# Kernel tuning notes

Hardware: AMD Instinct MI355X
Metric: run time of the kernel (lower is better)

## Reference

```python
import jax, jax.numpy as jnp
import numpy as np

N = 4096            # nodes
LMAX = 6
NUM_COEF = (LMAX + 1) ** 2   # 49 SH coefficients
RES = 18            # S2 grid resolution (lat = lon = 18)
C = 128             # num_channels


def setup_inputs() -> dict:
    key = jax.random.key(0)
    k1, k2, k3, k4 = jax.random.split(key, 4)
    return {
        "inputs": jax.random.normal(k1, (N, NUM_COEF, 2 * C), dtype=jnp.float32),
        "scalars": jax.random.normal(k2, (N, 3 * C), dtype=jnp.float32),
        # SO3Grid projection matrices (precomputed SH-basis grids in the real module)
        "to_grid_mat": jax.random.normal(k3, (RES, RES, NUM_COEF), dtype=jnp.float32) / np.sqrt(NUM_COEF).astype(np.float32),
        "from_grid_mat": jax.random.normal(k4, (RES, RES, NUM_COEF), dtype=jnp.float32) / np.float32(RES),
    }


def reference(inputs, scalars, to_grid_mat, from_grid_mat):
    # inputs:  [N, (lmax+1)^2, 2C]; scalars: [N, 3C]
    n, k, c2 = inputs.shape
    s = scalars[:, None, :]                       # [N, 1, 3C]
    # Type-0 path part 1: SwiGLU on first 2C scalars -> [N, 1, C]
    a, b = jnp.split(s[..., :c2], 2, axis=-1)
    output_scalars = jax.nn.silu(a) * b
    # Type-0 path part 2: sigmoid gate on last C scalars -> [N, 1, C]
    gate_scalars = jax.nn.sigmoid(s[..., c2:])
    # Type-L path: project to S2 grid -> [N, RES, RES, 2C]
    x_grid = jnp.einsum('pqi,nic->npqc', to_grid_mat, inputs)
    # chunk-multiply gating (self tensor product) -> [N, RES, RES, C]
    x1, x2 = jnp.split(x_grid, 2, axis=-1)
    x_grid = x1 * x2
    # project back to SH coefficients -> [N, (lmax+1)^2, C]
    output_vectors = jnp.einsum('pqi,npqc->nic', from_grid_mat, x_grid)
    output_vectors = output_vectors * gate_scalars
    # merge: add SwiGLU scalars onto the l=0 component
    return output_vectors.at[:, 0:1, :].add(output_scalars)
```

## Files before the change

### kernel.cpp

```cpp
#include <hip/hip_runtime.h>


#define KC    49
#define PQ    324
#define NPX   12544
#define OUTK  6272
#define NTILE 11
#define TROWS 325
#define TCOLS 68
#define FROWS 50
#define FCOLS 356
#define TTOT  (TROWS * TCOLS)
#define FTOT  (FROWS * FCOLS)
#define WTOT  (TTOT + FTOT)
#define WPAD  39904

typedef __attribute__((ext_vector_type(8)))  short bf16x8;
typedef __attribute__((ext_vector_type(4)))  short bf16x4;
typedef __attribute__((ext_vector_type(16))) float f32x16;
typedef __attribute__((ext_vector_type(4)))  unsigned int u32x4;

__device__ __forceinline__ unsigned int cvtpk_bf16(float lo, float hi) {
    unsigned int r;
    asm("v_cvt_pk_bf16_f32 %0, %1, %2" : "=v"(r) : "v"(lo), "v"(hi));
    return r;
}
__device__ __forceinline__ unsigned short f2bf(float f) {
    unsigned u = __builtin_bit_cast(unsigned, f);
    return (unsigned short)((u + 0x7FFFu + ((u >> 16) & 1u)) >> 16);
}
__device__ __forceinline__ bf16x8 ld8(const unsigned short* p) {
    const bf16x4 lo = *(const bf16x4*)p;
    const bf16x4 hi = *(const bf16x4*)(p + 4);
    bf16x8 r;
    r[0] = lo[0]; r[1] = lo[1]; r[2] = lo[2]; r[3] = lo[3];
    r[4] = hi[0]; r[5] = hi[1]; r[6] = hi[2]; r[7] = hi[3];
    return r;
}

__global__ void prep_kernel(const float* __restrict__ Tg, const float* __restrict__ Fg,
                            unsigned short* __restrict__ W)
{
    const int idx = blockIdx.x * 256 + threadIdx.x;
    if (idx < TTOT) {
        const int r = idx / TCOLS, i = idx % TCOLS;
        const float v = (r < PQ && i < KC) ? Tg[r * KC + i] : 0.0f;
        W[idx] = f2bf(v);
    } else if (idx < WPAD) {
        float v = 0.0f;
        if (idx < WTOT) {
            const int idx2 = idx - TTOT;
            const int k = idx2 / FCOLS, p = idx2 % FCOLS;
            if (k < KC && p < PQ) v = Fg[p * KC + k];
        }
        W[idx] = f2bf(v);
    }
}

__global__ __launch_bounds__(512, 2)
void s2_fused(const float* __restrict__ X,
              const float* __restrict__ S,
              const unsigned short* __restrict__ W,
              float* __restrict__ out,
              int nit)
{
    __shared__ __align__(16) unsigned short lds[WPAD];

    const int tid = threadIdx.x;
    for (int idx = tid; idx < WPAD / 8; idx += 512) {
        const u32x4 v = *(const u32x4*)(W + (size_t)idx * 8);
        *(u32x4*)(lds + (size_t)idx * 8) = v;
    }
    __syncthreads();

    const int w  = tid >> 6;
    const int l  = tid & 63;
    const int cl = l & 31;
    const int hb = l >> 5;
    const int cs = w >> 1;
    const int nw = w & 1;

    const unsigned short* tw  = lds;
    const unsigned short* fw0 = lds + TTOT + (size_t)cl * FCOLS;
    const unsigned short* fw1 = lds + TTOT + (size_t)min(cl + 32, KC) * FCOLS;

    const int nbase = blockIdx.x * (2 * nit) + nw;

    float fr[2][4][8];
    float sraw0, sraw1, sraw2;

    {
        const float* xp = X + (size_t)nbase * NPX + 32 * cs + cl;
#pragma unroll
        for (int xi = 0; xi < 2; ++xi)
#pragma unroll
        for (int st = 0; st < 4; ++st)
#pragma unroll
        for (int j = 0; j < 8; ++j) {
            const int i = 16 * st + 8 * hb + j;
            fr[xi][st][j] = (i < KC) ? xp[128 * xi + (size_t)i * 256] : 0.0f;
        }
        const float* sp = S + (size_t)nbase * 384 + 32 * cs + cl;
        sraw0 = sp[0]; sraw1 = sp[128]; sraw2 = sp[256];
    }

    for (int it = 0; it < nit; ++it) {
        const int n = nbase + 2 * it;

        const float sg  = 1.0f / (1.0f + __expf(-sraw2));
        const float osc = (sraw0 / (1.0f + __expf(-sraw0))) * sraw1;

        bf16x8 bx[2][4];
#pragma unroll
        for (int xi = 0; xi < 2; ++xi)
#pragma unroll
        for (int st = 0; st < 4; ++st) {
            u32x4 d;
#pragma unroll
            for (int p = 0; p < 4; ++p)
                d[p] = cvtpk_bf16(fr[xi][st][2 * p], fr[xi][st][2 * p + 1]);
            bx[xi][st] = __builtin_bit_cast(bf16x8, d);
        }

        {
            const int n2 = nbase + 2 * ((it + 1 < nit) ? it + 1 : it);
            const float* xp = X + (size_t)n2 * NPX + 32 * cs + cl;
#pragma unroll
            for (int xi = 0; xi < 2; ++xi)
#pragma unroll
            for (int st = 0; st < 4; ++st)
#pragma unroll
            for (int j = 0; j < 8; ++j) {
                const int i = 16 * st + 8 * hb + j;
                fr[xi][st][j] = (i < KC) ? xp[128 * xi + (size_t)i * 256] : 0.0f;
            }
            const float* sp = S + (size_t)n2 * 384 + 32 * cs + cl;
            sraw0 = sp[0]; sraw1 = sp[128]; sraw2 = sp[256];
        }

        f32x16 accO0, accO1;
#pragma unroll
        for (int r = 0; r < 16; ++r) { accO0[r] = 0.0f; accO1[r] = 0.0f; }

#pragma unroll 2
        for (int t = 0; t < NTILE; ++t) {
            const int trow = min(32 * t + cl, 324);
            const unsigned short* twt = tw + trow * TCOLS + 8 * hb;
            const bf16x8 ta0 = ld8(twt);
            const bf16x8 ta1 = ld8(twt + 16);
            const bf16x8 ta2 = ld8(twt + 32);
            const bf16x8 ta3 = ld8(twt + 48);
            const int fcol = 32 * t + 8 * hb;
            const bf16x8 fa00 = ld8(fw0 + fcol);
            const bf16x8 fa01 = ld8(fw0 + fcol + 16);
            const bf16x8 fa10 = ld8(fw1 + fcol);
            const bf16x8 fa11 = ld8(fw1 + fcol + 16);

            f32x16 ac0, ac1;
#pragma unroll
            for (int r = 0; r < 16; ++r) { ac0[r] = 0.0f; ac1[r] = 0.0f; }
            ac0 = __builtin_amdgcn_mfma_f32_32x32x16_bf16(ta0, bx[0][0], ac0, 0, 0, 0);
            ac1 = __builtin_amdgcn_mfma_f32_32x32x16_bf16(ta0, bx[1][0], ac1, 0, 0, 0);
            ac0 = __builtin_amdgcn_mfma_f32_32x32x16_bf16(ta1, bx[0][1], ac0, 0, 0, 0);
            ac1 = __builtin_amdgcn_mfma_f32_32x32x16_bf16(ta1, bx[1][1], ac1, 0, 0, 0);
            ac0 = __builtin_amdgcn_mfma_f32_32x32x16_bf16(ta2, bx[0][2], ac0, 0, 0, 0);
            ac1 = __builtin_amdgcn_mfma_f32_32x32x16_bf16(ta2, bx[1][2], ac1, 0, 0, 0);
            ac0 = __builtin_amdgcn_mfma_f32_32x32x16_bf16(ta3, bx[0][3], ac0, 0, 0, 0);
            ac1 = __builtin_amdgcn_mfma_f32_32x32x16_bf16(ta3, bx[1][3], ac1, 0, 0, 0);

            unsigned int q0 = cvtpk_bf16(ac0[0]  * ac1[0],  ac0[1]  * ac1[1]);
            unsigned int q1 = cvtpk_bf16(ac0[2]  * ac1[2],  ac0[3]  * ac1[3]);
            unsigned int q2 = cvtpk_bf16(ac0[4]  * ac1[4],  ac0[5]  * ac1[5]);
            unsigned int q3 = cvtpk_bf16(ac0[6]  * ac1[6],  ac0[7]  * ac1[7]);
            unsigned int q4 = cvtpk_bf16(ac0[8]  * ac1[8],  ac0[9]  * ac1[9]);
            unsigned int q5 = cvtpk_bf16(ac0[10] * ac1[10], ac0[11] * ac1[11]);
            unsigned int q6 = cvtpk_bf16(ac0[12] * ac1[12], ac0[13] * ac1[13]);
            unsigned int q7 = cvtpk_bf16(ac0[14] * ac1[14], ac0[15] * ac1[15]);

            asm("v_permlane32_swap_b32 %0, %1" : "+v"(q0), "+v"(q2));
            asm("v_permlane32_swap_b32 %0, %1" : "+v"(q1), "+v"(q3));
            asm("v_permlane32_swap_b32 %0, %1" : "+v"(q4), "+v"(q6));
            asm("v_permlane32_swap_b32 %0, %1" : "+v"(q5), "+v"(q7));
            u32x4 b0v, b1v;
            b0v[0] = q0; b0v[1] = q1; b0v[2] = q2; b0v[3] = q3;
            b1v[0] = q4; b1v[1] = q5; b1v[2] = q6; b1v[3] = q7;
            const bf16x8 bg0 = __builtin_bit_cast(bf16x8, b0v);
            const bf16x8 bg1 = __builtin_bit_cast(bf16x8, b1v);

            accO0 = __builtin_amdgcn_mfma_f32_32x32x16_bf16(fa00, bg0, accO0, 0, 0, 0);
            accO1 = __builtin_amdgcn_mfma_f32_32x32x16_bf16(fa10, bg0, accO1, 0, 0, 0);
            accO0 = __builtin_amdgcn_mfma_f32_32x32x16_bf16(fa01, bg1, accO0, 0, 0, 0);
            accO1 = __builtin_amdgcn_mfma_f32_32x32x16_bf16(fa11, bg1, accO1, 0, 0, 0);
        }

        float* op = out + (size_t)n * OUTK + 32 * cs + cl;
#pragma unroll
        for (int r = 0; r < 16; ++r) {
            const int k0 = (r & 3) + 8 * (r >> 2) + 4 * hb;
            float v = sg * accO0[r];
            if (k0 == 0) v += osc;
            op[(size_t)k0 * 128] = v;
            const int k1 = 32 + k0;
            if (k1 < KC) op[(size_t)k1 * 128] = sg * accO1[r];
        }
    }
}

extern "C" void kernel_launch(void* const* d_in, const int* in_sizes, int n_in,
                              void* d_out, int out_size, void* d_ws, size_t ws_size,
                              hipStream_t stream) {
    const float* inputs  = (const float*)d_in[0];
    const float* scalars = (const float*)d_in[1];
    const float* Tg      = (const float*)d_in[2];
    const float* Fg      = (const float*)d_in[3];
    float* outp          = (float*)d_out;

    unsigned short* W = (unsigned short*)d_ws;

    const int N = in_sizes[1] / 384;
    hipLaunchKernelGGL(prep_kernel, dim3((WPAD + 255) / 256), dim3(256), 0, stream,
                       Tg, Fg, W);

    const int nit  = 4;
    const int grid = N / (2 * nit);
    hipLaunchKernelGGL(s2_fused, dim3(grid), dim3(512), 0, stream,
                       inputs, scalars, W, outp, nit);
}
```

Before: 94.48 us.

## Drop cross-iteration input prefetch to cut registers and raise occupancy to 4 blocks

Removes the register-held prefetch of the next node's 64 input floats and instead loads each node's inputs inside the iteration, in chunks that are converted to bf16 as they arrive. The from-grid weight LDS loads move after the first GEMM stage to shorten their live range. Launch bounds go from 2 to 4 blocks per CU so more waves can hide memory latency. The trade-off is that global load latency is no longer overlapped with the previous node's MFMA work inside a wave. Fitting the register budget for 4 blocks could also cause spills, and the 78KB LDS footprint may not actually allow 4 blocks per CU.

```diff
diff --git a/kernel.cpp b/kernel.cpp
--- a/kernel.cpp
+++ b/kernel.cpp
@@ -57,7 +57,7 @@
     }
 }
 
-__global__ __launch_bounds__(512, 2)
+__global__ __launch_bounds__(512, 4)
 void s2_fused(const float* __restrict__ X,
               const float* __restrict__ S,
               const unsigned short* __restrict__ W,
@@ -86,56 +86,45 @@
 
     const int nbase = blockIdx.x * (2 * nit) + nw;
 
-    float fr[2][4][8];
-    float sraw0, sraw1, sraw2;
-
-    {
-        const float* xp = X + (size_t)nbase * NPX + 32 * cs + cl;
-#pragma unroll
-        for (int xi = 0; xi < 2; ++xi)
-#pragma unroll
-        for (int st = 0; st < 4; ++st)
-#pragma unroll
-        for (int j = 0; j < 8; ++j) {
-            const int i = 16 * st + 8 * hb + j;
-            fr[xi][st][j] = (i < KC) ? xp[128 * xi + (size_t)i * 256] : 0.0f;
-        }
-        const float* sp = S + (size_t)nbase * 384 + 32 * cs + cl;
-        sraw0 = sp[0]; sraw1 = sp[128]; sraw2 = sp[256];
-    }
-
     for (int it = 0; it < nit; ++it) {
         const int n = nbase + 2 * it;
 
+        const float* xp = X + (size_t)n * NPX + 32 * cs + cl;
+        const float* sp = S + (size_t)n * 384 + 32 * cs + cl;
+        const float sraw0 = sp[0], sraw1 = sp[128], sraw2 = sp[256];
         const float sg  = 1.0f / (1.0f + __expf(-sraw2));
         const float osc = (sraw0 / (1.0f + __expf(-sraw0))) * sraw1;
 
         bf16x8 bx[2][4];
-#pragma unroll
-        for (int xi = 0; xi < 2; ++xi)
-#pragma unroll
-        for (int st = 0; st < 4; ++st) {
-            u32x4 d;
-#pragma unroll
-            for (int p = 0; p < 4; ++p)
-                d[p] = cvtpk_bf16(fr[xi][st][2 * p], fr[xi][st][2 * p + 1]);
-            bx[xi][st] = __builtin_bit_cast(bf16x8, d);
-        }
-
         {
-            const int n2 = nbase + 2 * ((it + 1 < nit) ? it + 1 : it);
-            const float* xp = X + (size_t)n2 * NPX + 32 * cs + cl;
+            float ch[4][16];
 #pragma unroll
             for (int xi = 0; xi < 2; ++xi)
 #pragma unroll
-            for (int st = 0; st < 4; ++st)
-#pragma unroll
             for (int j = 0; j < 8; ++j) {
-                const int i = 16 * st + 8 * hb + j;
-                fr[xi][st][j] = (i < KC) ? xp[128 * xi + (size_t)i * 256] : 0.0f;
+                const int i = 8 * hb + j;
+                ch[0][8 * xi + j] = (i < KC) ? xp[128 * xi + (size_t)i * 256] : 0.0f;
             }
-            const float* sp = S + (size_t)n2 * 384 + 32 * cs + cl;
-            sraw0 = sp[0]; sraw1 = sp[128]; sraw2 = sp[256];
+#pragma unroll
+            for (int st = 0; st < 4; ++st) {
+                if (st < 3) {
+#pragma unroll
+                    for (int xi = 0; xi < 2; ++xi)
+#pragma unroll
+                    for (int j = 0; j < 8; ++j) {
+                        const int i = 16 * (st + 1) + 8 * hb + j;
+                        ch[st + 1][8 * xi + j] = (i < KC) ? xp[128 * xi + (size_t)i * 256] : 0.0f;
+                    }
+                }
+#pragma unroll
+                for (int xi = 0; xi < 2; ++xi) {
+                    u32x4 d;
+#pragma unroll
+                    for (int p = 0; p < 4; ++p)
+                        d[p] = cvtpk_bf16(ch[st][8 * xi + 2 * p], ch[st][8 * xi + 2 * p + 1]);
+                    bx[xi][st] = __builtin_bit_cast(bf16x8, d);
+                }
+            }
         }
 
         f32x16 accO0, accO1;
@@ -150,11 +139,6 @@
             const bf16x8 ta1 = ld8(twt + 16);
             const bf16x8 ta2 = ld8(twt + 32);
             const bf16x8 ta3 = ld8(twt + 48);
-            const int fcol = 32 * t + 8 * hb;
-            const bf16x8 fa00 = ld8(fw0 + fcol);
-            const bf16x8 fa01 = ld8(fw0 + fcol + 16);
-            const bf16x8 fa10 = ld8(fw1 + fcol);
-            const bf16x8 fa11 = ld8(fw1 + fcol + 16);
 
             f32x16 ac0, ac1;
 #pragma unroll
@@ -187,6 +171,12 @@
             const bf16x8 bg0 = __builtin_bit_cast(bf16x8, b0v);
             const bf16x8 bg1 = __builtin_bit_cast(bf16x8, b1v);
 
+            const int fcol = 32 * t + 8 * hb;
+            const bf16x8 fa00 = ld8(fw0 + fcol);
+            const bf16x8 fa01 = ld8(fw0 + fcol + 16);
+            const bf16x8 fa10 = ld8(fw1 + fcol);
+            const bf16x8 fa11 = ld8(fw1 + fcol + 16);
+
             accO0 = __builtin_amdgcn_mfma_f32_32x32x16_bf16(fa00, bg0, accO0, 0, 0, 0);
             accO1 = __builtin_amdgcn_mfma_f32_32x32x16_bf16(fa10, bg0, accO1, 0, 0, 0);
             accO0 = __builtin_amdgcn_mfma_f32_32x32x16_bf16(fa01, bg1, accO0, 0, 0, 0);
```

After: 115.5 us. 22.2% more time.
